# Performance work log

Measured on AMD Instinct MI355X. Metric: run time of the kernel, lower is better.

## Reference

```python
import jax, jax.numpy as jnp
import numpy as np

N_COLS = 4096
N_ROWS = 4096
H = 64          # args.hidden1
S = 2           # per-edge supp feature count (cv_supp/vc_supp dim 0)
S_VO = 2        # vo_supp feature dim
S_CO = 2        # co_supp feature dim
EDGE_DENSITY = 0.03


def setup_inputs() -> dict:
    key = jax.random.key(0)
    ks = jax.random.split(key, 20)
    col_hidden = jax.random.normal(ks[0], (N_COLS, H), jnp.float32)
    row_hidden = jax.random.normal(ks[1], (N_ROWS, H), jnp.float32)
    obj_hidden = jax.random.normal(ks[2], (1, H), jnp.float32)
    # sparse bipartite adjacency encoded in supp[0] != 0 (as in the TF code)
    mask = jax.random.bernoulli(ks[3], EDGE_DENSITY, (N_ROWS, N_COLS))
    cv_supp = jax.random.normal(ks[4], (S, N_ROWS, N_COLS), jnp.float32) * mask[None]
    vc_supp = jnp.transpose(cv_supp, (0, 2, 1))  # [S, ncols, nrows]
    vo_supp = jax.random.normal(ks[5], (N_COLS, S_VO), jnp.float32)
    co_supp = jax.random.normal(ks[6], (N_ROWS, S_CO), jnp.float32)
    w = 0.05
    W_vo = jax.random.normal(ks[7], (2 * H, H), jnp.float32) * w
    W_oc = jax.random.normal(ks[8], (2 * H, H), jnp.float32) * w
    W_vc = jax.random.normal(ks[9], (2 * H, H), jnp.float32) * w
    W_co = jax.random.normal(ks[10], (2 * H, H), jnp.float32) * w
    W_ov = jax.random.normal(ks[11], (2 * H, H), jnp.float32) * w
    W_cv = jax.random.normal(ks[12], (2 * H, H), jnp.float32) * w
    # attention scorer nets: Dense(concat_dim -> 1) + sigmoid
    w_attn_vo = jax.random.normal(ks[13], (2 * H + S_VO, 1), jnp.float32) * 0.1
    b_attn_vo = jnp.zeros((), jnp.float32)
    w_attn_co = jax.random.normal(ks[14], (2 * H + S_CO, 1), jnp.float32) * 0.1
    b_attn_co = jnp.zeros((), jnp.float32)
    # pairwise attn nets decomposed into [col | supp | row] weight slices
    w_cv_col = jax.random.normal(ks[15], (H,), jnp.float32) * 0.1
    w_cv_supp = jax.random.normal(ks[16], (S,), jnp.float32) * 0.1
    w_cv_row = jax.random.normal(ks[17], (H,), jnp.float32) * 0.1
    b_cv = jnp.zeros((), jnp.float32)
    w_vc_row = jax.random.normal(ks[18], (H,), jnp.float32) * 0.1
    w_vc_supp = jax.random.normal(ks[19], (S,), jnp.float32) * 0.1
    w_vc_col = jax.random.normal(jax.random.fold_in(key, 99), (H,), jnp.float32) * 0.1
    b_vc = jnp.zeros((), jnp.float32)
    return dict(col_hidden=col_hidden, row_hidden=row_hidden, obj_hidden=obj_hidden,
                cv_supp=cv_supp, vc_supp=vc_supp, vo_supp=vo_supp, co_supp=co_supp,
                W_vo=W_vo, W_oc=W_oc, W_vc=W_vc, W_co=W_co, W_ov=W_ov, W_cv=W_cv,
                w_attn_vo=w_attn_vo, b_attn_vo=b_attn_vo,
                w_attn_co=w_attn_co, b_attn_co=b_attn_co,
                w_cv_col=w_cv_col, w_cv_supp=w_cv_supp, w_cv_row=w_cv_row, b_cv=b_cv,
                w_vc_row=w_vc_row, w_vc_supp=w_vc_supp, w_vc_col=w_vc_col, b_vc=b_vc)


def _forward(col_hidden, row_hidden, obj_hidden, cv_supp, vc_supp, vo_supp, co_supp,
             W_vo, W_oc, W_vc, W_co, W_ov, W_cv,
             w_attn_vo, b_attn_vo, w_attn_co, b_attn_co,
             w_cv_col, w_cv_supp, w_cv_row, b_cv,
             w_vc_row, w_vc_supp, w_vc_col, b_vc):
    act = jax.nn.relu
    ncols, nrows = col_hidden.shape[0], row_hidden.shape[0]
    # ---- v -> o: attend over all columns, update obj node ----
    vo_in = jnp.concatenate([col_hidden, vo_supp,
                             jnp.broadcast_to(obj_hidden, (ncols, H))], axis=1)
    a_vo = jax.nn.sigmoid(vo_in @ w_attn_vo + b_attn_vo)          # [ncols, 1]
    v_o_out = a_vo.T @ col_hidden                                  # [1, H]
    obj = act(jnp.concatenate([obj_hidden, v_o_out], axis=1) @ W_vo)
    # ---- v -> c: per-row ragged neighbor attention, vectorized via masked pairwise scores ----
    nbr_cv = cv_supp[0] != 0                                       # [nrows, ncols]
    logits_cv = ((row_hidden @ w_cv_row)[:, None]
                 + (col_hidden @ w_cv_col)[None, :]
                 + jnp.einsum('snc,s->nc', cv_supp, w_cv_supp) + b_cv)
    score_cv = jnp.where(nbr_cv, jax.nn.sigmoid(logits_cv), 0.0)   # [nrows, ncols]
    v_out = score_cv @ col_hidden                                  # [nrows, H]
    o_c_out = act(jnp.concatenate([jnp.broadcast_to(obj, (nrows, H)), row_hidden], axis=1) @ W_oc)
    row_next = act(jnp.concatenate([o_c_out, v_out], axis=1) @ W_vc)
    # ---- c -> o ----
    co_in = jnp.concatenate([row_next, co_supp,
                             jnp.broadcast_to(obj, (nrows, H))], axis=1)
    a_co = jax.nn.sigmoid(co_in @ w_attn_co + b_attn_co)           # [nrows, 1]
    c_o_out = a_co.T @ row_next                                    # [1, H]
    obj = act(jnp.concatenate([obj, c_o_out], axis=1) @ W_co)
    # ---- c -> v ----
    nbr_vc = vc_supp[0] != 0                                       # [ncols, nrows]
    logits_vc = ((col_hidden @ w_vc_col)[:, None]
                 + (row_next @ w_vc_row)[None, :]
                 + jnp.einsum('scn,s->cn', vc_supp, w_vc_supp) + b_vc)
    score_vc = jnp.where(nbr_vc, jax.nn.sigmoid(logits_vc), 0.0)   # [ncols, nrows]
    c_out = score_vc @ row_next                                    # [ncols, H]
    o_v_out = act(jnp.concatenate([jnp.broadcast_to(obj, (ncols, H)), col_hidden], axis=1) @ W_ov)
    col_next = act(jnp.concatenate([o_v_out, c_out], axis=1) @ W_cv)
    return col_next, row_next, obj


def reference(col_hidden, row_hidden, obj_hidden, cv_supp, vc_supp, vo_supp, co_supp,
              W_vo, W_oc, W_vc, W_co, W_ov, W_cv,
              w_attn_vo, b_attn_vo, w_attn_co, b_attn_co,
              w_cv_col, w_cv_supp, w_cv_row, b_cv,
              w_vc_row, w_vc_supp, w_vc_col, b_vc):
    col_next, row_next, obj = _forward(
        col_hidden, row_hidden, obj_hidden, cv_supp, vc_supp, vo_supp, co_supp,
        W_vo, W_oc, W_vc, W_co, W_ov, W_cv,
        w_attn_vo, b_attn_vo, w_attn_co, b_attn_co,
        w_cv_col, w_cv_supp, w_cv_row, b_cv,
        w_vc_row, w_vc_supp, w_vc_col, b_vc)
    # original layer also passes the supp tensors through unchanged
    return (col_next, row_next, obj, cv_supp, vc_supp, vo_supp, co_supp)
```

## Files before the change

### kernel.cpp

```cpp
#include <hip/hip_runtime.h>
#include <math.h>

typedef float f4 __attribute__((ext_vector_type(4)));

#define PLANE (4096*4096)

#define OUT_COL 0
#define OUT_ROW 262144
#define OUT_OBJ 524288
#define OUT_CV  524352
#define OUT_VC  34078784
#define OUT_VO  67633216
#define OUT_CO  67641408

#define WS_VO_P 0
#define WS_CO_P 1024
#define WS_OBJ1 2048
#define WS_RDCV 2112
#define WS_CDCV 6208
#define WS_RDVC 10304
#define WS_CDVC 14400
#define WS_PART 18496

__device__ __forceinline__ float sigf(float x) {
    return 1.0f / (1.0f + __expf(-x));
}

#define SSWZ(row, f4col) (((row) << 6) + ((f4col) ^ ((((row) >> 2) & 3) << 1)))

__device__ __forceinline__ void attn_body(
    int blk, int t, const float* __restrict__ X, const float* __restrict__ supp,
    const float* __restrict__ obj, const float* __restrict__ wat,
    const float* __restrict__ bat, float* __restrict__ accP,
    const float* __restrict__ wextra, float* __restrict__ dextra,
    float* sA, float* sAcc)
{
    const int i = blk * 256 + t;
    float od = 0.f;
    for (int h = 0; h < 64; ++h) od += obj[h] * wat[66 + h];
    float x = bat[0] + od + supp[i*2] * wat[64] + supp[i*2+1] * wat[65];
    const f4* Xr = (const f4*)(X + i*64);
    f4 xd = 0.f, dd = 0.f;
    #pragma unroll
    for (int q = 0; q < 16; ++q) {
        f4 xv = Xr[q];
        xd += xv * ((const f4*)wat)[q];
        if (wextra) dd += xv * ((const f4*)wextra)[q];
    }
    x += xd.x + xd.y + xd.z + xd.w;
    if (dextra) dextra[i] = dd.x + dd.y + dd.z + dd.w;
    sA[t] = sigf(x);
    if (t < 64) sAcc[t] = 0.f;
    __syncthreads();
    const int w = t >> 6, h = t & 63;
    const int base = blk * 256 + w * 64;
    float partial = 0.f;
    for (int j = 0; j < 64; ++j)
        partial += sA[w*64 + j] * X[(base + j)*64 + h];
    atomicAdd(&sAcc[h], partial);
    __syncthreads();
    if (t < 64) accP[blk*64 + t] = sAcc[t];
}

__global__ __launch_bounds__(256) void k_front(
    const float* __restrict__ col_hidden, const float* __restrict__ row_hidden,
    const float* __restrict__ w_cv_col, const float* __restrict__ w_vc_col,
    const float* __restrict__ w_cv_row,
    float* __restrict__ cdcv, float* __restrict__ cdvc, float* __restrict__ rdcv,
    const float* __restrict__ vo_supp, const float* __restrict__ co_supp,
    float* __restrict__ out_vo, float* __restrict__ out_co,
    const float* __restrict__ obj_hidden, const float* __restrict__ w_attn_vo,
    const float* __restrict__ b_attn_vo, float* __restrict__ voP)
{
    __shared__ float sA[256];
    __shared__ float sAcc[64];
    const int t = threadIdx.x;
    if (blockIdx.x < 3072) {
        const int gw = blockIdx.x * 4 + (t >> 6);
        const int lane = t & 63;
        const int which = gw >> 12;
        const int row = gw & 4095;
        const float* x; const float* w; float* dst;
        if (which == 0)      { x = col_hidden; w = w_cv_col; dst = cdcv; }
        else if (which == 1) { x = col_hidden; w = w_vc_col; dst = cdvc; }
        else                 { x = row_hidden; w = w_cv_row; dst = rdcv; }
        float v = x[row * 64 + lane] * w[lane];
        #pragma unroll
        for (int off = 32; off; off >>= 1) v += __shfl_down(v, off, 64);
        if (lane == 0) dst[row] = v;
        return;
    }
    if (blockIdx.x < 3088) {
        const int idx = (blockIdx.x - 3072) * 256 + t;
        if (idx < 2048) ((f4*)out_vo)[idx] = ((const f4*)vo_supp)[idx];
        else            ((f4*)out_co)[idx - 2048] = ((const f4*)co_supp)[idx - 2048];
        return;
    }
    attn_body(blockIdx.x - 3088, t, col_hidden, vo_supp, obj_hidden,
              w_attn_vo, b_attn_vo, voP, nullptr, nullptr, sA, sAcc);
}

__global__ __launch_bounds__(256) void k_attn(
    const float* __restrict__ X, const float* __restrict__ supp,
    const float* __restrict__ obj, const float* __restrict__ wat,
    const float* __restrict__ bat, float* __restrict__ accP,
    const float* __restrict__ wextra, float* __restrict__ dextra)
{
    __shared__ float sA[256];
    __shared__ float sAcc[64];
    attn_body(blockIdx.x, threadIdx.x, X, supp, obj, wat, bat, accP,
              wextra, dextra, sA, sAcc);
}

__global__ __launch_bounds__(256, 2) void k_big(
    const float* __restrict__ supp0, const float* __restrict__ supp1,
    const float* __restrict__ Bm,
    const float* __restrict__ rdot, const float* __restrict__ cdot,
    const float* __restrict__ wsup, const float* __restrict__ bias,
    float* __restrict__ part, float* __restrict__ pass0, float* __restrict__ pass1,
    const float* __restrict__ objL, const float* __restrict__ objRp,
    const float* __restrict__ Wobj, float* __restrict__ objDst)
{
    __shared__ __align__(16) f4 sS[4096];
    __shared__ __align__(16) float sB[64][64];
    const int t = threadIdx.x;

    if (blockIdx.x == 1024) {
        float* rsum = (float*)sS;
        if (t < 64) {
            float r = 0.f;
            for (int b = 0; b < 16; ++b) r += objRp[b*64 + t];
            rsum[t] = r;
        }
        __syncthreads();
        if (t < 64) {
            float acc = 0.f;
            for (int k = 0; k < 64; ++k) acc += objL[k] * Wobj[k*64 + t];
            for (int k = 0; k < 64; ++k) acc += rsum[k] * Wobj[(64+k)*64 + t];
            objDst[t] = fmaxf(acc, 0.f);
        }
        return;
    }

    const int bi = blockIdx.x >> 4;
    const int bj = blockIdx.x & 15;
    const int i0 = bi * 64;
    const int jt0 = bj * 256;
    const float w0 = wsup[0], w1 = wsup[1], bv = bias[0];

    const int srow = t >> 6;
    const int sf4  = t & 63;
    const int scol = sf4 * 4;
    const f4 cd = *(const f4*)(cdot + jt0 + scol);
    #pragma unroll 4
    for (int q = 0; q < 16; ++q) {
        const int row = q*4 + srow;
        const size_t idx = (size_t)(i0 + row) * 4096 + jt0 + scol;
        f4 a0 = *(const f4*)(supp0 + idx);
        f4 a1 = *(const f4*)(supp1 + idx);
        __builtin_nontemporal_store(a0, (f4*)(pass0 + idx));
        __builtin_nontemporal_store(a1, (f4*)(pass1 + idx));
        const float rd = rdot[i0 + row];
        f4 lg = rd + cd + w0*a0 + w1*a1 + bv;
        f4 s;
        s.x = (a0.x != 0.f) ? sigf(lg.x) : 0.f;
        s.y = (a0.y != 0.f) ? sigf(lg.y) : 0.f;
        s.z = (a0.z != 0.f) ? sigf(lg.z) : 0.f;
        s.w = (a0.w != 0.f) ? sigf(lg.w) : 0.f;
        sS[SSWZ(row, sf4)] = s;
    }
    {
        const f4* src = (const f4*)(Bm + (size_t)jt0 * 64);
        f4* dstp = (f4*)&sB[0][0];
        dstp[t]       = src[t];
        dstp[t + 256] = src[t + 256];
        dstp[t + 512] = src[t + 512];
        dstp[t + 768] = src[t + 768];
    }
    __syncthreads();

    const int ilb = t >> 4;
    const int h0  = (t & 15) * 4;
    f4 acc0 = 0.f, acc1 = 0.f, acc2 = 0.f, acc3 = 0.f;
    for (int q4 = 0; q4 < 4; ++q4) {
        if (q4) {
            __syncthreads();
            const f4* src = (const f4*)(Bm + (size_t)(jt0 + q4*64) * 64);
            f4* dstp = (f4*)&sB[0][0];
            dstp[t]       = src[t];
            dstp[t + 256] = src[t + 256];
            dstp[t + 512] = src[t + 512];
            dstp[t + 768] = src[t + 768];
            __syncthreads();
        }
        const int c4 = q4 * 16;
        #pragma unroll
        for (int jf = 0; jf < 16; ++jf) {
            const int jj = jf * 4;
            f4 b0 = *(const f4*)&sB[jj + 0][h0];
            f4 b1 = *(const f4*)&sB[jj + 1][h0];
            f4 b2 = *(const f4*)&sB[jj + 2][h0];
            f4 b3 = *(const f4*)&sB[jj + 3][h0];
            { f4 s = sS[SSWZ(ilb*4 + 0, c4 + jf)]; acc0 += s.x*b0 + s.y*b1 + s.z*b2 + s.w*b3; }
            { f4 s = sS[SSWZ(ilb*4 + 1, c4 + jf)]; acc1 += s.x*b0 + s.y*b1 + s.z*b2 + s.w*b3; }
            { f4 s = sS[SSWZ(ilb*4 + 2, c4 + jf)]; acc2 += s.x*b0 + s.y*b1 + s.z*b2 + s.w*b3; }
            { f4 s = sS[SSWZ(ilb*4 + 3, c4 + jf)]; acc3 += s.x*b0 + s.y*b1 + s.z*b2 + s.w*b3; }
        }
    }
    float* pb = part + (size_t)bj * 262144 + (size_t)i0 * 64;
    *(f4*)(pb + (ilb*4 + 0)*64 + h0) = acc0;
    *(f4*)(pb + (ilb*4 + 1)*64 + h0) = acc1;
    *(f4*)(pb + (ilb*4 + 2)*64 + h0) = acc2;
    *(f4*)(pb + (ilb*4 + 3)*64 + h0) = acc3;
}

__global__ __launch_bounds__(256) void k_mlp2(
    const float* __restrict__ objx, const float* __restrict__ base,
    const float* __restrict__ W1, const float* __restrict__ part,
    const float* __restrict__ W2, float* __restrict__ dst)
{
    __shared__ float mid[4][64];
    __shared__ float accs[4][64];
    const int t = threadIdx.x, w = t >> 6, h = t & 63;
    const int n = blockIdx.x * 4 + w;
    float v = 0.f;
    #pragma unroll
    for (int j = 0; j < 16; ++j) v += part[(size_t)j * 262144 + n*64 + h];
    accs[w][h] = v;
    float m = 0.f;
    for (int k = 0; k < 64; ++k) m += objx[k] * W1[k*64 + h];
    for (int k = 0; k < 64; ++k) m += base[n*64 + k] * W1[(64+k)*64 + h];
    mid[w][h] = fmaxf(m, 0.f);
    __syncthreads();
    float o = 0.f;
    for (int k = 0; k < 64; ++k) o += mid[w][k] * W2[k*64 + h];
    for (int k = 0; k < 64; ++k) o += accs[w][k] * W2[(64+k)*64 + h];
    dst[n*64 + h] = fmaxf(o, 0.f);
}

extern "C" void kernel_launch(void* const* d_in, const int* in_sizes, int n_in,
                              void* d_out, int out_size, void* d_ws, size_t ws_size,
                              hipStream_t stream)
{
    const float* col_hidden = (const float*)d_in[0];
    const float* row_hidden = (const float*)d_in[1];
    const float* obj_hidden = (const float*)d_in[2];
    const float* cv_supp    = (const float*)d_in[3];
    const float* vc_supp    = (const float*)d_in[4];
    const float* vo_supp    = (const float*)d_in[5];
    const float* co_supp    = (const float*)d_in[6];
    const float* W_vo       = (const float*)d_in[7];
    const float* W_oc       = (const float*)d_in[8];
    const float* W_vc       = (const float*)d_in[9];
    const float* W_co       = (const float*)d_in[10];
    const float* W_ov       = (const float*)d_in[11];
    const float* W_cv       = (const float*)d_in[12];
    const float* w_attn_vo  = (const float*)d_in[13];
    const float* b_attn_vo  = (const float*)d_in[14];
    const float* w_attn_co  = (const float*)d_in[15];
    const float* b_attn_co  = (const float*)d_in[16];
    const float* w_cv_col   = (const float*)d_in[17];
    const float* w_cv_supp  = (const float*)d_in[18];
    const float* w_cv_row   = (const float*)d_in[19];
    const float* b_cv       = (const float*)d_in[20];
    const float* w_vc_row   = (const float*)d_in[21];
    const float* w_vc_supp  = (const float*)d_in[22];
    const float* w_vc_col   = (const float*)d_in[23];
    const float* b_vc       = (const float*)d_in[24];

    float* out = (float*)d_out;
    float* ws  = (float*)d_ws;

    k_front<<<3104, 256, 0, stream>>>(col_hidden, row_hidden, w_cv_col, w_vc_col, w_cv_row,
                                      ws + WS_CDCV, ws + WS_CDVC, ws + WS_RDCV,
                                      vo_supp, co_supp, out + OUT_VO, out + OUT_CO,
                                      obj_hidden, w_attn_vo, b_attn_vo, ws + WS_VO_P);
    k_big<<<1025, 256, 0, stream>>>(cv_supp, cv_supp + PLANE, col_hidden,
                                    ws + WS_RDCV, ws + WS_CDCV, w_cv_supp, b_cv,
                                    ws + WS_PART, out + OUT_CV, out + OUT_CV + PLANE,
                                    obj_hidden, ws + WS_VO_P, W_vo, ws + WS_OBJ1);
    k_mlp2<<<1024, 256, 0, stream>>>(ws + WS_OBJ1, row_hidden, W_oc, ws + WS_PART, W_vc,
                                     out + OUT_ROW);
    k_attn<<<16, 256, 0, stream>>>(out + OUT_ROW, co_supp, ws + WS_OBJ1, w_attn_co, b_attn_co,
                                   ws + WS_CO_P, w_vc_row, ws + WS_RDVC);
    k_big<<<1025, 256, 0, stream>>>(vc_supp, vc_supp + PLANE, out + OUT_ROW,
                                    ws + WS_CDVC, ws + WS_RDVC, w_vc_supp, b_vc,
                                    ws + WS_PART, out + OUT_VC, out + OUT_VC + PLANE,
                                    ws + WS_OBJ1, ws + WS_CO_P, W_co, out + OUT_OBJ);
    k_mlp2<<<1024, 256, 0, stream>>>(out + OUT_OBJ, col_hidden, W_ov, ws + WS_PART, W_cv,
                                     out + OUT_COL);
}
```

Before: 606.5 us.

## Stage supp tiles via direct global-to-LDS loads and halve column tile width

The big attention-matmul kernel now loads both supp planes and the B tile straight into LDS with global_load_lds, instead of going through registers. The column tile shrinks from 256 to 128, so twice as many blocks run and the partial-sum count doubles to 32, which the reduction kernel now sums. The passthrough stores move from nontemporal to ordinary stores, and the score tile reuses the supp LDS buffer. This aims to raise memory-level parallelism on a bandwidth-bound pass, at the cost of more partial-sum traffic and an extra barrier between load and compute.

```diff
diff --git a/kernel.cpp b/kernel.cpp
--- a/kernel.cpp
+++ b/kernel.cpp
@@ -26,7 +26,13 @@
     return 1.0f / (1.0f + __expf(-x));
 }
 
-#define SSWZ(row, f4col) (((row) << 6) + ((f4col) ^ ((((row) >> 2) & 3) << 1)))
+#define AS1 __attribute__((address_space(1)))
+#define AS3 __attribute__((address_space(3)))
+__device__ __forceinline__ void gl_lds16(const float* g, float* l) {
+    __builtin_amdgcn_global_load_lds((const AS1 void*)g, (AS3 void*)l, 16, 0, 0);
+}
+
+#define SSWZ_F4C(row, f4c) ((f4c) ^ ((((row) >> 2) & 3) << 1))
 
 __device__ __forceinline__ void attn_body(
     int blk, int t, const float* __restrict__ X, const float* __restrict__ supp,
@@ -121,97 +127,92 @@
     const float* __restrict__ objL, const float* __restrict__ objRp,
     const float* __restrict__ Wobj, float* __restrict__ objDst)
 {
-    __shared__ __align__(16) f4 sS[4096];
-    __shared__ __align__(16) float sB[64][64];
+    __shared__ __align__(16) float lds0[64*128];
+    __shared__ __align__(16) float lds1[64*128];
     const int t = threadIdx.x;
 
-    if (blockIdx.x == 1024) {
-        float* rsum = (float*)sS;
+    if (blockIdx.x == 2048) {
         if (t < 64) {
             float r = 0.f;
             for (int b = 0; b < 16; ++b) r += objRp[b*64 + t];
-            rsum[t] = r;
+            lds0[t] = r;
         }
         __syncthreads();
         if (t < 64) {
             float acc = 0.f;
             for (int k = 0; k < 64; ++k) acc += objL[k] * Wobj[k*64 + t];
-            for (int k = 0; k < 64; ++k) acc += rsum[k] * Wobj[(64+k)*64 + t];
+            for (int k = 0; k < 64; ++k) acc += lds0[k] * Wobj[(64+k)*64 + t];
             objDst[t] = fmaxf(acc, 0.f);
         }
         return;
     }
 
-    const int bi = blockIdx.x >> 4;
-    const int bj = blockIdx.x & 15;
+    const int bi = blockIdx.x >> 5;
+    const int bj = blockIdx.x & 31;
     const int i0 = bi * 64;
-    const int jt0 = bj * 256;
+    const int jt0 = bj * 128;
+    const int w = t >> 6, lane = t & 63;
     const float w0 = wsup[0], w1 = wsup[1], bv = bias[0];
 
-    const int srow = t >> 6;
-    const int sf4  = t & 63;
-    const int scol = sf4 * 4;
-    const f4 cd = *(const f4*)(cdot + jt0 + scol);
+    for (int k = 0; k < 8; ++k) {
+        const int p = w * 8 + k;
+        const size_t g = (size_t)(i0 + 2*p + (lane >> 5)) * 4096 + jt0 + (lane & 31) * 4;
+        gl_lds16(supp0 + g, lds0 + p * 256);
+        gl_lds16(supp1 + g, lds1 + p * 256);
+    }
+    __syncthreads();
+
+    {
+        const int f4c = lane & 31;
+        const f4 cd = *(const f4*)(cdot + jt0 + f4c * 4);
+        for (int q = 0; q < 8; ++q) {
+            const int p = q * 4 + w;
+            const int row = 2 * p + (lane >> 5);
+            f4 a0 = *(const f4*)(lds0 + p * 256 + lane * 4);
+            f4 a1 = *(const f4*)(lds1 + p * 256 + lane * 4);
+            const size_t g = (size_t)(i0 + row) * 4096 + jt0 + f4c * 4;
+            *(f4*)(pass0 + g) = a0;
+            *(f4*)(pass1 + g) = a1;
+            const float rd = rdot[i0 + row];
+            f4 lg = rd + cd + w0 * a0 + w1 * a1 + bv;
+            f4 s;
+            s.x = (a0.x != 0.f) ? sigf(lg.x) : 0.f;
+            s.y = (a0.y != 0.f) ? sigf(lg.y) : 0.f;
+            s.z = (a0.z != 0.f) ? sigf(lg.z) : 0.f;
+            s.w = (a0.w != 0.f) ? sigf(lg.w) : 0.f;
+            *(f4*)(lds0 + row * 128 + SSWZ_F4C(row, f4c) * 4) = s;
+        }
+    }
+    __syncthreads();
+
+    for (int k = 0; k < 8; ++k) {
+        const int c = w * 8 + k;
+        gl_lds16(Bm + (size_t)(jt0 + c * 4) * 64 + lane * 4, lds1 + c * 256);
+    }
+    __syncthreads();
+
+    const int ilb = t >> 4;
+    const int hf4 = t & 15;
+    const int sw  = (ilb & 3) << 1;
+    f4 acc0 = 0.f, acc1 = 0.f, acc2 = 0.f, acc3 = 0.f;
     #pragma unroll 4
-    for (int q = 0; q < 16; ++q) {
-        const int row = q*4 + srow;
-        const size_t idx = (size_t)(i0 + row) * 4096 + jt0 + scol;
-        f4 a0 = *(const f4*)(supp0 + idx);
-        f4 a1 = *(const f4*)(supp1 + idx);
-        __builtin_nontemporal_store(a0, (f4*)(pass0 + idx));
-        __builtin_nontemporal_store(a1, (f4*)(pass1 + idx));
-        const float rd = rdot[i0 + row];
-        f4 lg = rd + cd + w0*a0 + w1*a1 + bv;
-        f4 s;
-        s.x = (a0.x != 0.f) ? sigf(lg.x) : 0.f;
-        s.y = (a0.y != 0.f) ? sigf(lg.y) : 0.f;
-        s.z = (a0.z != 0.f) ? sigf(lg.z) : 0.f;
-        s.w = (a0.w != 0.f) ? sigf(lg.w) : 0.f;
-        sS[SSWZ(row, sf4)] = s;
-    }
-    {
-        const f4* src = (const f4*)(Bm + (size_t)jt0 * 64);
-        f4* dstp = (f4*)&sB[0][0];
-        dstp[t]       = src[t];
-        dstp[t + 256] = src[t + 256];
-        dstp[t + 512] = src[t + 512];
-        dstp[t + 768] = src[t + 768];
-    }
-    __syncthreads();
-
-    const int ilb = t >> 4;
-    const int h0  = (t & 15) * 4;
-    f4 acc0 = 0.f, acc1 = 0.f, acc2 = 0.f, acc3 = 0.f;
-    for (int q4 = 0; q4 < 4; ++q4) {
-        if (q4) {
-            __syncthreads();
-            const f4* src = (const f4*)(Bm + (size_t)(jt0 + q4*64) * 64);
-            f4* dstp = (f4*)&sB[0][0];
-            dstp[t]       = src[t];
-            dstp[t + 256] = src[t + 256];
-            dstp[t + 512] = src[t + 512];
-            dstp[t + 768] = src[t + 768];
-            __syncthreads();
-        }
-        const int c4 = q4 * 16;
-        #pragma unroll
-        for (int jf = 0; jf < 16; ++jf) {
-            const int jj = jf * 4;
-            f4 b0 = *(const f4*)&sB[jj + 0][h0];
-            f4 b1 = *(const f4*)&sB[jj + 1][h0];
-            f4 b2 = *(const f4*)&sB[jj + 2][h0];
-            f4 b3 = *(const f4*)&sB[jj + 3][h0];
-            { f4 s = sS[SSWZ(ilb*4 + 0, c4 + jf)]; acc0 += s.x*b0 + s.y*b1 + s.z*b2 + s.w*b3; }
-            { f4 s = sS[SSWZ(ilb*4 + 1, c4 + jf)]; acc1 += s.x*b0 + s.y*b1 + s.z*b2 + s.w*b3; }
-            { f4 s = sS[SSWZ(ilb*4 + 2, c4 + jf)]; acc2 += s.x*b0 + s.y*b1 + s.z*b2 + s.w*b3; }
-            { f4 s = sS[SSWZ(ilb*4 + 3, c4 + jf)]; acc3 += s.x*b0 + s.y*b1 + s.z*b2 + s.w*b3; }
-        }
+    for (int jf = 0; jf < 32; ++jf) {
+        const int jj = jf * 4;
+        f4 b0 = *(const f4*)(lds1 + (jj + 0) * 64 + hf4 * 4);
+        f4 b1 = *(const f4*)(lds1 + (jj + 1) * 64 + hf4 * 4);
+        f4 b2 = *(const f4*)(lds1 + (jj + 2) * 64 + hf4 * 4);
+        f4 b3 = *(const f4*)(lds1 + (jj + 3) * 64 + hf4 * 4);
+        const int sf = (jf ^ sw) * 4;
+        { f4 s = *(const f4*)(lds0 + (ilb*4 + 0) * 128 + sf); acc0 += s.x*b0 + s.y*b1 + s.z*b2 + s.w*b3; }
+        { f4 s = *(const f4*)(lds0 + (ilb*4 + 1) * 128 + sf); acc1 += s.x*b0 + s.y*b1 + s.z*b2 + s.w*b3; }
+        { f4 s = *(const f4*)(lds0 + (ilb*4 + 2) * 128 + sf); acc2 += s.x*b0 + s.y*b1 + s.z*b2 + s.w*b3; }
+        { f4 s = *(const f4*)(lds0 + (ilb*4 + 3) * 128 + sf); acc3 += s.x*b0 + s.y*b1 + s.z*b2 + s.w*b3; }
     }
     float* pb = part + (size_t)bj * 262144 + (size_t)i0 * 64;
-    *(f4*)(pb + (ilb*4 + 0)*64 + h0) = acc0;
-    *(f4*)(pb + (ilb*4 + 1)*64 + h0) = acc1;
-    *(f4*)(pb + (ilb*4 + 2)*64 + h0) = acc2;
-    *(f4*)(pb + (ilb*4 + 3)*64 + h0) = acc3;
+    *(f4*)(pb + (ilb*4 + 0)*64 + hf4*4) = acc0;
+    *(f4*)(pb + (ilb*4 + 1)*64 + hf4*4) = acc1;
+    *(f4*)(pb + (ilb*4 + 2)*64 + hf4*4) = acc2;
+    *(f4*)(pb + (ilb*4 + 3)*64 + hf4*4) = acc3;
 }
 
 __global__ __launch_bounds__(256) void k_mlp2(
@@ -224,8 +225,8 @@
     const int t = threadIdx.x, w = t >> 6, h = t & 63;
     const int n = blockIdx.x * 4 + w;
     float v = 0.f;
-    #pragma unroll
-    for (int j = 0; j < 16; ++j) v += part[(size_t)j * 262144 + n*64 + h];
+    #pragma unroll 8
+    for (int j = 0; j < 32; ++j) v += part[(size_t)j * 262144 + n*64 + h];
     accs[w][h] = v;
     float m = 0.f;
     for (int k = 0; k < 64; ++k) m += objx[k] * W1[k*64 + h];
@@ -275,7 +276,7 @@
                                       ws + WS_CDCV, ws + WS_CDVC, ws + WS_RDCV,
                                       vo_supp, co_supp, out + OUT_VO, out + OUT_CO,
                                       obj_hidden, w_attn_vo, b_attn_vo, ws + WS_VO_P);
-    k_big<<<1025, 256, 0, stream>>>(cv_supp, cv_supp + PLANE, col_hidden,
+    k_big<<<2049, 256, 0, stream>>>(cv_supp, cv_supp + PLANE, col_hidden,
                                     ws + WS_RDCV, ws + WS_CDCV, w_cv_supp, b_cv,
                                     ws + WS_PART, out + OUT_CV, out + OUT_CV + PLANE,
                                     obj_hidden, ws + WS_VO_P, W_vo, ws + WS_OBJ1);
@@ -283,7 +284,7 @@
                                      out + OUT_ROW);
     k_attn<<<16, 256, 0, stream>>>(out + OUT_ROW, co_supp, ws + WS_OBJ1, w_attn_co, b_attn_co,
                                    ws + WS_CO_P, w_vc_row, ws + WS_RDVC);
-    k_big<<<1025, 256, 0, stream>>>(vc_supp, vc_supp + PLANE, out + OUT_ROW,
+    k_big<<<2049, 256, 0, stream>>>(vc_supp, vc_supp + PLANE, out + OUT_ROW,
                                     ws + WS_CDVC, ws + WS_RDVC, w_vc_supp, b_vc,
                                     ws + WS_PART, out + OUT_VC, out + OUT_VC + PLANE,
                                     ws + WS_OBJ1, ws + WS_CO_P, W_co, out + OUT_OBJ);
```

Result: faster. 577.2 us (-4.8%).
